# Kernel optimization log

Hardware: AMD Instinct MI355X
Metric: run time of the kernel (lower is better)

The kernel has to match this reference:

```python
import jax, jax.numpy as jnp
import numpy as np

N = 100000          # number of nodes
E = 128             # embedding size
NUM_LAYERS = 4
SMOOTH = 12.0       # MAXIMUM_SMOOTHNESS
RELATIONS = [("at", 2), ("clear", 1), ("on", 2)]  # sorted, as in module
ATOM_COUNTS = {"at": 150000, "clear": 150000, "on": 150000}


def mish(x):
    return x * jnp.tanh(jax.nn.softplus(x))


def _linear_init(k, din, dout):
    s = 1.0 / np.sqrt(din)
    kw, kb = jax.random.split(k)
    w = jax.random.uniform(kw, (din, dout), jnp.float32, -s, s)
    b = jax.random.uniform(kb, (dout,), jnp.float32, -s, s)
    return w, b


def setup_inputs() -> dict:
    key = jax.random.key(0)
    ks = iter(jax.random.split(key, 64))
    inp = {}
    inp["node_embeddings"] = jax.random.normal(next(ks), (N, E), jnp.float32)
    for name, ar in RELATIONS:
        inp[f"atoms_{name}"] = jax.random.randint(
            next(ks), (ATOM_COUNTS[name] * ar,), 0, N, dtype=jnp.int32)
        d = ar * E
        inp[f"w_in_{name}"], inp[f"b_in_{name}"] = _linear_init(next(ks), d, d)
        inp[f"w_out_{name}"], inp[f"b_out_{name}"] = _linear_init(next(ks), d, d)
    # update MLP: Linear(2E, 2E) -> mish -> Linear(2E, E)
    inp["w_u_in"], inp["b_u_in"] = _linear_init(next(ks), 2 * E, 2 * E)
    inp["w_u_out"], inp["b_u_out"] = _linear_init(next(ks), 2 * E, E)
    return inp


def _forward(node_embeddings, atoms, params):
    w_u_in, b_u_in, w_u_out, b_u_out = params["update"]

    def layer(h):
        msgs, idxs = [], []
        for name, ar in RELATIONS:
            w_in, b_in, w_out, b_out = params[name]
            av = atoms[name]                              # [A*ar] node indices
            x = h[av].reshape(-1, ar * E)                 # gather -> [A, ar*E]
            y = x + (mish(x @ w_in + b_in) @ w_out + b_out)  # residual MLP
            msgs.append(y.reshape(-1, E))
            idxs.append(av)
        msg = jnp.concatenate(msgs, 0)                    # [T, E]
        idx = jnp.concatenate(idxs, 0)                    # [T]
        # smooth-max aggregation (max offsets are not differentiated)
        seg_max = jax.ops.segment_max(msg, idx, num_segments=N)
        seg_max = jnp.where(jnp.isfinite(seg_max), seg_max, 0.0)  # empty -> 0 (include_self=False on zeros)
        seg_max = jax.lax.stop_gradient(seg_max)
        exps = jnp.exp(SMOOTH * (msg - seg_max[idx]))
        exps_sum = jax.ops.segment_sum(exps, idx, num_segments=N) + 1e-16
        max_msg = jnp.log(exps_sum) / SMOOTH + seg_max
        upd_in = jnp.concatenate([max_msg, h], axis=1)    # [N, 2E]
        upd = mish(upd_in @ w_u_in + b_u_in) @ w_u_out + b_u_out
        return h + upd                                    # outer residual

    h = node_embeddings
    for _ in range(NUM_LAYERS):
        h = layer(h)
    return h


def reference(node_embeddings, atoms_at, atoms_clear, atoms_on,
              w_in_at, b_in_at, w_out_at, b_out_at,
              w_in_clear, b_in_clear, w_out_clear, b_out_clear,
              w_in_on, b_in_on, w_out_on, b_out_on,
              w_u_in, b_u_in, w_u_out, b_u_out):
    atoms = {"at": atoms_at, "clear": atoms_clear, "on": atoms_on}
    params = {
        "at": (w_in_at, b_in_at, w_out_at, b_out_at),
        "clear": (w_in_clear, b_in_clear, w_out_clear, b_out_clear),
        "on": (w_in_on, b_in_on, w_out_on, b_out_on),
        "update": (w_u_in, b_u_in, w_u_out, b_u_out),
    }
    return _forward(node_embeddings, atoms, params)
```

## Files before the change

kernel.cpp:

```cpp
#include <hip/hip_runtime.h>
#include <hip/hip_bf16.h>
#include <math.h>

#define NNODES 100000
#define EDIM 128
#define TSLOTS 750000
#define NB 391

typedef __bf16 bf16x8 __attribute__((ext_vector_type(8)));
typedef __bf16 bf16x4 __attribute__((ext_vector_type(4)));
typedef float f32x4 __attribute__((ext_vector_type(4)));

#define T_SCALE 17.312340490667562f
#define INV_SCALE 0.05776226504666211f
#define EMPTY_V (-3.0701134f)

__device__ __forceinline__ float mishf(float x) {
  float u = __expf(fminf(x, 15.f));
  float num = u * (u + 2.f);
  return x * num * __builtin_amdgcn_rcpf(num + 2.f);
}

__device__ __forceinline__ double exp12t(float t) {
  t = fmaxf(t, -20000.f);
  float ti = floorf(t);
  float m = exp2f(t - ti);
  int ei = (int)ti;
  ei = ei < -1000 ? -1000 : (ei > 1000 ? 1000 : ei);
  return (double)m * __longlong_as_double(((long long)(1023 + ei)) << 52);
}

__device__ __forceinline__ float logS12(double S) {
  if (!(S > 0.0)) return EMPTY_V;
  long long b = __double_as_longlong(S);
  int e2 = (int)((b >> 52) & 0x7FF) - 1023;
  float mf = __uint_as_float(0x3F800000u | (unsigned)((b >> 29) & 0x7FFFFF));
  return ((float)e2 + log2f(mf)) * INV_SCALE;
}

__global__ void k_sentinel(float* out, int n) {
  int i = blockIdx.x * 256 + threadIdx.x;
  if (i < n) out[i] = 1.0e6f;
}

__global__ void k_init(const float* __restrict__ h0, __bf16* __restrict__ hb, int n8) {
  int i = blockIdx.x * 256 + threadIdx.x;
  if (i >= n8) return;
  float4 f0 = ((const float4*)h0)[i * 2];
  float4 f1 = ((const float4*)h0)[i * 2 + 1];
  bf16x8 p = {(__bf16)f0.x, (__bf16)f0.y, (__bf16)f0.z, (__bf16)f0.w,
              (__bf16)f1.x, (__bf16)f1.y, (__bf16)f1.z, (__bf16)f1.w};
  *(bf16x8*)(hb + (size_t)i * 8) = p;
}

struct TransDesc {
  const float* src[8];
  __bf16* dst[8];
  int R[8];
  int C[8];
  int tstart[9];
};

__global__ void k_transpose_all(TransDesc td) {
  __shared__ float tile[32][33];
  int b = blockIdx.x;
  int m = 0;
  while (m < 7 && b >= td.tstart[m + 1]) m++;
  int t = b - td.tstart[m];
  int R = td.R[m], C = td.C[m];
  int tcols = C >> 5;
  int by = t / tcols, bx = t - by * tcols;
  int tx = threadIdx.x & 31, ty = threadIdx.x >> 5;
  const float* src = td.src[m];
  __bf16* dst = td.dst[m];
  for (int i = 0; i < 32; i += 8)
    tile[ty + i][tx] = src[(size_t)(by * 32 + ty + i) * C + bx * 32 + tx];
  __syncthreads();
  for (int i = 0; i < 32; i += 8)
    dst[(size_t)(bx * 32 + ty + i) * R + by * 32 + tx] = (__bf16)tile[tx][ty + i];
}

__device__ __forceinline__ int slot_node(int s, const int* at, const int* cl, const int* on) {
  if (s < 300000) return at[s];
  if (s < 450000) return cl[s - 300000];
  return on[s - 450000];
}

__global__ void k_count(const int* __restrict__ at, const int* __restrict__ cl,
                        const int* __restrict__ on, int* __restrict__ cnt) {
  int s = blockIdx.x * 256 + threadIdx.x;
  if (s >= TSLOTS) return;
  atomicAdd(&cnt[slot_node(s, at, cl, on)], 1);
}

__global__ void k_bsum(const int* __restrict__ cnt, int* __restrict__ bsum) {
  __shared__ int sm[256];
  int n = blockIdx.x * 256 + threadIdx.x;
  sm[threadIdx.x] = (n < NNODES) ? cnt[n] : 0;
  __syncthreads();
  for (int st = 128; st > 0; st >>= 1) {
    if (threadIdx.x < st) sm[threadIdx.x] += sm[threadIdx.x + st];
    __syncthreads();
  }
  if (threadIdx.x == 0) bsum[blockIdx.x] = sm[0];
}

__global__ void k_bscan(const int* __restrict__ bsum, int* __restrict__ bpre,
                        int* __restrict__ off) {
  __shared__ int sm[512];
  int t = threadIdx.x;
  int v = (t < NB) ? bsum[t] : 0;
  sm[t] = v;
  __syncthreads();
  for (int st = 1; st < 512; st <<= 1) {
    int x = (t >= st) ? sm[t - st] : 0;
    __syncthreads();
    sm[t] += x;
    __syncthreads();
  }
  if (t < NB) bpre[t] = sm[t] - v;
  if (t == NB - 1) off[NNODES] = sm[t];
}

__global__ void k_off(const int* __restrict__ cnt, const int* __restrict__ bpre,
                      int* __restrict__ off) {
  __shared__ int sm[256];
  int n = blockIdx.x * 256 + threadIdx.x;
  int v = (n < NNODES) ? cnt[n] : 0;
  sm[threadIdx.x] = v;
  __syncthreads();
  for (int st = 1; st < 256; st <<= 1) {
    int t = (threadIdx.x >= st) ? sm[threadIdx.x - st] : 0;
    __syncthreads();
    sm[threadIdx.x] += t;
    __syncthreads();
  }
  if (n < NNODES) off[n] = bpre[blockIdx.x] + sm[threadIdx.x] - v;
}

__global__ void k_fill(const int* __restrict__ at, const int* __restrict__ cl,
                       const int* __restrict__ on, const int* __restrict__ off,
                       int* __restrict__ cnt, int* __restrict__ perm) {
  int s = blockIdx.x * 256 + threadIdx.x;
  if (s >= TSLOTS) return;
  int node = slot_node(s, at, cl, on);
  int pos = atomicAdd(&cnt[node], -1) - 1;
  perm[s] = off[node] + pos;
}

__global__ __launch_bounds__(256, 4) void k_rel2(
    const float* __restrict__ hf, const __bf16* __restrict__ hb,
    const int* __restrict__ av,
    const __bf16* __restrict__ wt1, const float* __restrict__ b1,
    const __bf16* __restrict__ wt2, const float* __restrict__ b2,
    _Float16* __restrict__ msg, const int* __restrict__ permrel, int A) {
  __shared__ __align__(16) __bf16 xs[64][264];
  __shared__ int prm[128];
  const int tid = threadIdx.x;
  const int lane = tid & 63;
  const int w = tid >> 6;
  const int row0 = blockIdx.x * 64;

  if (tid < 128) {
    int i2 = row0 * 2 + tid;
    prm[tid] = (i2 < 2 * A) ? permrel[i2] : 0;
  }
  if (hb != nullptr) {
    for (int i = 0; i < 8; ++i) {
      int s = tid + i * 256;
      int r = s >> 5, o = s & 31;
      int a = row0 + r;
      uint4 v = {0, 0, 0, 0};
      if (a < A) {
        int node = av[2 * a + (o >> 4)];
        v = *(const uint4*)(hb + (size_t)node * 128 + (o & 15) * 8);
      }
      *(uint4*)&xs[r][o * 8] = v;
    }
  } else {
    for (int i = 0; i < 16; ++i) {
      int s = tid + i * 256;
      int r = s >> 6, o = s & 63;
      int a = row0 + r;
      float4 f = {0.f, 0.f, 0.f, 0.f};
      if (a < A) {
        int node = av[2 * a + (o >> 5)];
        f = *(const float4*)(hf + (size_t)node * 128 + (o & 31) * 4);
      }
      bf16x4 p = {(__bf16)f.x, (__bf16)f.y, (__bf16)f.z, (__bf16)f.w};
      *(bf16x4*)&xs[r][o * 4] = p;
    }
  }
  __syncthreads();

  const int lhi = lane >> 4, llo = lane & 15;
  const int cb = w * 64;

  f32x4 acc1[4][4];
#pragma unroll
  for (int rt = 0; rt < 4; rt++)
#pragma unroll
    for (int ct = 0; ct < 4; ct++) acc1[rt][ct] = (f32x4){0.f, 0.f, 0.f, 0.f};

#pragma unroll
  for (int kk = 0; kk < 8; ++kk) {
    int k = kk * 32 + lhi * 8;
    bf16x8 af[4], bfr[4];
#pragma unroll
    for (int rt = 0; rt < 4; rt++) af[rt] = *(const bf16x8*)&xs[rt * 16 + llo][k];
#pragma unroll
    for (int ct = 0; ct < 4; ct++)
      bfr[ct] = *(const bf16x8*)(wt1 + (size_t)(cb + ct * 16 + llo) * 256 + k);
#pragma unroll
    for (int rt = 0; rt < 4; rt++)
#pragma unroll
      for (int ct = 0; ct < 4; ct++)
        acc1[rt][ct] = __builtin_amdgcn_mfma_f32_16x16x32_bf16(af[rt], bfr[ct], acc1[rt][ct], 0, 0, 0);
  }
  __syncthreads();

  float b1v[4];
#pragma unroll
  for (int ct = 0; ct < 4; ct++) b1v[ct] = b1[cb + ct * 16 + llo];
#pragma unroll
  for (int rt = 0; rt < 4; rt++)
#pragma unroll
    for (int ct = 0; ct < 4; ct++)
#pragma unroll
      for (int i = 0; i < 4; i++)
        xs[rt * 16 + lhi * 4 + i][cb + ct * 16 + llo] = (__bf16)mishf(acc1[rt][ct][i] + b1v[ct]);
  __syncthreads();

  f32x4 acc2[4][4];
#pragma unroll
  for (int rt = 0; rt < 4; rt++)
#pragma unroll
    for (int ct = 0; ct < 4; ct++) acc2[rt][ct] = (f32x4){0.f, 0.f, 0.f, 0.f};

#pragma unroll
  for (int kk = 0; kk < 8; ++kk) {
    int k = kk * 32 + lhi * 8;
    bf16x8 af[4], bfr[4];
#pragma unroll
    for (int rt = 0; rt < 4; rt++) af[rt] = *(const bf16x8*)&xs[rt * 16 + llo][k];
#pragma unroll
    for (int ct = 0; ct < 4; ct++)
      bfr[ct] = *(const bf16x8*)(wt2 + (size_t)(cb + ct * 16 + llo) * 256 + k);
#pragma unroll
    for (int rt = 0; rt < 4; rt++)
#pragma unroll
      for (int ct = 0; ct < 4; ct++)
        acc2[rt][ct] = __builtin_amdgcn_mfma_f32_16x16x32_bf16(af[rt], bfr[ct], acc2[rt][ct], 0, 0, 0);
  }
  __syncthreads();

  float b2v[4];
#pragma unroll
  for (int ct = 0; ct < 4; ct++) b2v[ct] = b2[cb + ct * 16 + llo];
  ushort* zs = (ushort*)&xs[0][0];
#pragma unroll
  for (int rt = 0; rt < 4; rt++)
#pragma unroll
    for (int ct = 0; ct < 4; ct++)
#pragma unroll
      for (int i = 0; i < 4; i++) {
        int r = rt * 16 + lhi * 4 + i;
        int col = cb + ct * 16 + llo;
        union { ushort u; _Float16 f; } cv;
        cv.f = (_Float16)(acc2[rt][ct][i] + b2v[ct]);
        zs[r * 264 + col] = cv.u;
      }
  __syncthreads();

  for (int i = 0; i < 8; ++i) {
    int s = tid + i * 256;
    int sr = s >> 4;
    int c = s & 15;
    int a = row0 + (sr >> 1);
    if (a < A) {
      int rr = sr >> 1, c0 = (sr & 1) * 128 + c * 8;
      uint4 z = *(const uint4*)&zs[rr * 264 + c0];
      *(uint4*)(msg + (size_t)prm[sr] * 128 + c * 8) = z;
    }
  }
}

__global__ __launch_bounds__(256, 4) void k_rel1(
    const float* __restrict__ hf, const __bf16* __restrict__ hb,
    const int* __restrict__ av,
    const __bf16* __restrict__ wt1, const float* __restrict__ b1,
    const __bf16* __restrict__ wt2, const float* __restrict__ b2,
    _Float16* __restrict__ msg, const int* __restrict__ permrel, int A) {
  __shared__ __align__(16) __bf16 xs[64][136];
  __shared__ int prm[64];
  const int tid = threadIdx.x;
  const int lane = tid & 63;
  const int w = tid >> 6;
  const int row0 = blockIdx.x * 64;

  if (tid < 64) {
    int a = row0 + tid;
    prm[tid] = (a < A) ? permrel[a] : 0;
  }
  if (hb != nullptr) {
    for (int i = 0; i < 4; ++i) {
      int s = tid + i * 256;
      int r = s >> 4, o = s & 15;
      int a = row0 + r;
      uint4 v = {0, 0, 0, 0};
      if (a < A) {
        int node = av[a];
        v = *(const uint4*)(hb + (size_t)node * 128 + o * 8);
      }
      *(uint4*)&xs[r][o * 8] = v;
    }
  } else {
    for (int i = 0; i < 8; ++i) {
      int s = tid + i * 256;
      int r = s >> 5, o = s & 31;
      int a = row0 + r;
      float4 f = {0.f, 0.f, 0.f, 0.f};
      if (a < A) {
        int node = av[a];
        f = *(const float4*)(hf + (size_t)node * 128 + o * 4);
      }
      bf16x4 p = {(__bf16)f.x, (__bf16)f.y, (__bf16)f.z, (__bf16)f.w};
      *(bf16x4*)&xs[r][o * 4] = p;
    }
  }
  __syncthreads();

  const int lhi = lane >> 4, llo = lane & 15;
  const int cb = w * 32;

  f32x4 acc1[4][2];
#pragma unroll
  for (int rt = 0; rt < 4; rt++)
#pragma unroll
    for (int ct = 0; ct < 2; ct++) acc1[rt][ct] = (f32x4){0.f, 0.f, 0.f, 0.f};

#pragma unroll
  for (int kk = 0; kk < 4; ++kk) {
    int k = kk * 32 + lhi * 8;
    bf16x8 af[4], bfr[2];
#pragma unroll
    for (int rt = 0; rt < 4; rt++) af[rt] = *(const bf16x8*)&xs[rt * 16 + llo][k];
#pragma unroll
    for (int ct = 0; ct < 2; ct++)
      bfr[ct] = *(const bf16x8*)(wt1 + (size_t)(cb + ct * 16 + llo) * 128 + k);
#pragma unroll
    for (int rt = 0; rt < 4; rt++)
#pragma unroll
      for (int ct = 0; ct < 2; ct++)
        acc1[rt][ct] = __builtin_amdgcn_mfma_f32_16x16x32_bf16(af[rt], bfr[ct], acc1[rt][ct], 0, 0, 0);
  }
  __syncthreads();

  float b1v[2];
#pragma unroll
  for (int ct = 0; ct < 2; ct++) b1v[ct] = b1[cb + ct * 16 + llo];
#pragma unroll
  for (int rt = 0; rt < 4; rt++)
#pragma unroll
    for (int ct = 0; ct < 2; ct++)
#pragma unroll
      for (int i = 0; i < 4; i++)
        xs[rt * 16 + lhi * 4 + i][cb + ct * 16 + llo] = (__bf16)mishf(acc1[rt][ct][i] + b1v[ct]);
  __syncthreads();

  f32x4 acc2[4][2];
#pragma unroll
  for (int rt = 0; rt < 4; rt++)
#pragma unroll
    for (int ct = 0; ct < 2; ct++) acc2[rt][ct] = (f32x4){0.f, 0.f, 0.f, 0.f};

#pragma unroll
  for (int kk = 0; kk < 4; ++kk) {
    int k = kk * 32 + lhi * 8;
    bf16x8 af[4], bfr[2];
#pragma unroll
    for (int rt = 0; rt < 4; rt++) af[rt] = *(const bf16x8*)&xs[rt * 16 + llo][k];
#pragma unroll
    for (int ct = 0; ct < 2; ct++)
      bfr[ct] = *(const bf16x8*)(wt2 + (size_t)(cb + ct * 16 + llo) * 128 + k);
#pragma unroll
    for (int rt = 0; rt < 4; rt++)
#pragma unroll
      for (int ct = 0; ct < 2; ct++)
        acc2[rt][ct] = __builtin_amdgcn_mfma_f32_16x16x32_bf16(af[rt], bfr[ct], acc2[rt][ct], 0, 0, 0);
  }
  __syncthreads();

  float b2v[2];
#pragma unroll
  for (int ct = 0; ct < 2; ct++) b2v[ct] = b2[cb + ct * 16 + llo];
  ushort* zs = (ushort*)&xs[0][0];
#pragma unroll
  for (int rt = 0; rt < 4; rt++)
#pragma unroll
    for (int ct = 0; ct < 2; ct++)
#pragma unroll
      for (int i = 0; i < 4; i++) {
        int r = rt * 16 + lhi * 4 + i;
        int col = cb + ct * 16 + llo;
        union { ushort u; _Float16 f; } cv;
        cv.f = (_Float16)(acc2[rt][ct][i] + b2v[ct]);
        zs[r * 136 + col] = cv.u;
      }
  __syncthreads();

  for (int i = 0; i < 4; ++i) {
    int s = tid + i * 256;
    int sr = s >> 4;
    int c = s & 15;
    int a = row0 + sr;
    if (a < A) {
      uint4 z = *(const uint4*)&zs[sr * 136 + c * 8];
      *(uint4*)(msg + (size_t)prm[sr] * 128 + c * 8) = z;
    }
  }
}

__global__ __launch_bounds__(256, 8) void k_agg(
    const _Float16* __restrict__ msg, const int* __restrict__ off,
    const float* __restrict__ hf, const __bf16* __restrict__ hb,
    __bf16* __restrict__ mm) {
  __shared__ int offs[33];
  const int tid = threadIdx.x;
  const int lane = tid & 63;
  const int w = tid >> 6;
  const int node0 = blockIdx.x * 32;
  if (tid < 33) {
    int n = node0 + tid;
    offs[tid] = off[n < NNODES ? n : NNODES];
  }
  __syncthreads();

  const int fl = lane & 31;
  const int p = lane >> 5;
  const _Float16* mb = msg + fl * 4;

#pragma unroll 1
  for (int j = 0; j < 8; ++j) {
    int n = node0 + w * 8 + j;
    if (n >= NNODES) break;
    float h0, h1, h2, h3;
    if (hb != nullptr) {
      bf16x4 hq = *(const bf16x4*)(hb + (size_t)n * 128 + fl * 4);
      h0 = (float)hq[0]; h1 = (float)hq[1]; h2 = (float)hq[2]; h3 = (float)hq[3];
    } else {
      float4 hq = *(const float4*)(hf + (size_t)n * 128 + fl * 4);
      h0 = hq.x; h1 = hq.y; h2 = hq.z; h3 = hq.w;
    }
    int beg = offs[w * 8 + j];
    int deg = offs[w * 8 + j + 1] - beg;
    double S0 = 0.0, S1 = 0.0, S2 = 0.0, S3 = 0.0;
#pragma unroll 1
    for (int d = 0; d < deg; d += 2) {
      int rp = d + p;
      int rc = rp < deg - 1 ? rp : deg - 1;
      uint2 v = *(const uint2*)(mb + (size_t)(beg + rc) * 128);
      if (rp >= deg) { v.x = 0xFC00FC00u; v.y = 0xFC00FC00u; }
      union { uint2 u; _Float16 f[4]; } q;
      q.u = v;
      S0 += exp12t(((float)q.f[0] + h0) * T_SCALE);
      S1 += exp12t(((float)q.f[1] + h1) * T_SCALE);
      S2 += exp12t(((float)q.f[2] + h2) * T_SCALE);
      S3 += exp12t(((float)q.f[3] + h3) * T_SCALE);
    }
    S0 += __shfl_xor(S0, 32);
    S1 += __shfl_xor(S1, 32);
    S2 += __shfl_xor(S2, 32);
    S3 += __shfl_xor(S3, 32);
    if (p == 0) {
      bf16x4 r;
      r[0] = (__bf16)logS12(S0);
      r[1] = (__bf16)logS12(S1);
      r[2] = (__bf16)logS12(S2);
      r[3] = (__bf16)logS12(S3);
      *(bf16x4*)(mm + (size_t)n * 128 + fl * 4) = r;
    }
  }
}

__global__ __launch_bounds__(256, 4) void k_mlp(
    const float* __restrict__ hin, const __bf16* __restrict__ mm,
    const __bf16* __restrict__ wt1, const float* __restrict__ b1,
    const __bf16* __restrict__ wt2, const float* __restrict__ b2,
    float* __restrict__ hout, __bf16* __restrict__ hbout) {
  __shared__ __align__(16) __bf16 xs[64][264];
  const int tid = threadIdx.x;
  const int lane = tid & 63;
  const int w = tid >> 6;
  const int node0 = blockIdx.x * 64;

  for (int i = 0; i < 4; ++i) {
    int s = tid + i * 256;
    int r = s >> 4, o = s & 15;
    int n = node0 + r;
    uint4 v = {0, 0, 0, 0};
    if (n < NNODES) v = *(const uint4*)(mm + (size_t)n * 128 + o * 8);
    *(uint4*)&xs[r][o * 8] = v;
  }
  for (int i = 0; i < 8; ++i) {
    int s = tid + i * 256;
    int r = s >> 5, o = s & 31;
    int n = node0 + r;
    float4 f = {0.f, 0.f, 0.f, 0.f};
    if (n < NNODES) f = *(const float4*)(hin + (size_t)n * 128 + o * 4);
    bf16x4 p = {(__bf16)f.x, (__bf16)f.y, (__bf16)f.z, (__bf16)f.w};
    *(bf16x4*)&xs[r][128 + o * 4] = p;
  }
  __syncthreads();

  const int lhi = lane >> 4, llo = lane & 15;
  const int cb = w * 64;

  f32x4 acc1[4][4];
#pragma unroll
  for (int rt = 0; rt < 4; rt++)
#pragma unroll
    for (int ct = 0; ct < 4; ct++) acc1[rt][ct] = (f32x4){0.f, 0.f, 0.f, 0.f};

#pragma unroll
  for (int kk = 0; kk < 8; ++kk) {
    int k = kk * 32 + lhi * 8;
    bf16x8 af[4], bfr[4];
#pragma unroll
    for (int rt = 0; rt < 4; rt++) af[rt] = *(const bf16x8*)&xs[rt * 16 + llo][k];
#pragma unroll
    for (int ct = 0; ct < 4; ct++)
      bfr[ct] = *(const bf16x8*)(wt1 + (size_t)(cb + ct * 16 + llo) * 256 + k);
#pragma unroll
    for (int rt = 0; rt < 4; rt++)
#pragma unroll
      for (int ct = 0; ct < 4; ct++)
        acc1[rt][ct] = __builtin_amdgcn_mfma_f32_16x16x32_bf16(af[rt], bfr[ct], acc1[rt][ct], 0, 0, 0);
  }
  __syncthreads();

  float b1v[4];
#pragma unroll
  for (int ct = 0; ct < 4; ct++) b1v[ct] = b1[cb + ct * 16 + llo];
#pragma unroll
  for (int rt = 0; rt < 4; rt++)
#pragma unroll
    for (int ct = 0; ct < 4; ct++)
#pragma unroll
      for (int i = 0; i < 4; i++)
        xs[rt * 16 + lhi * 4 + i][cb + ct * 16 + llo] = (__bf16)mishf(acc1[rt][ct][i] + b1v[ct]);
  __syncthreads();

  const int cb2 = w * 32;
  f32x4 acc2[4][2];
#pragma unroll
  for (int rt = 0; rt < 4; rt++)
#pragma unroll
    for (int ct = 0; ct < 2; ct++) acc2[rt][ct] = (f32x4){0.f, 0.f, 0.f, 0.f};

#pragma unroll
  for (int kk = 0; kk < 8; ++kk) {
    int k = kk * 32 + lhi * 8;
    bf16x8 af[4], bfr[2];
#pragma unroll
    for (int rt = 0; rt < 4; rt++) af[rt] = *(const bf16x8*)&xs[rt * 16 + llo][k];
#pragma unroll
    for (int ct = 0; ct < 2; ct++)
      bfr[ct] = *(const bf16x8*)(wt2 + (size_t)(cb2 + ct * 16 + llo) * 256 + k);
#pragma unroll
    for (int rt = 0; rt < 4; rt++)
#pragma unroll
      for (int ct = 0; ct < 2; ct++)
        acc2[rt][ct] = __builtin_amdgcn_mfma_f32_16x16x32_bf16(af[rt], bfr[ct], acc2[rt][ct], 0, 0, 0);
  }

  float b2v[2];
#pragma unroll
  for (int ct = 0; ct < 2; ct++) b2v[ct] = b2[cb2 + ct * 16 + llo];
#pragma unroll
  for (int rt = 0; rt < 4; rt++)
#pragma unroll
    for (int i = 0; i < 4; i++) {
      int r = rt * 16 + lhi * 4 + i;
      int n = node0 + r;
      if (n >= NNODES) continue;
#pragma unroll
      for (int ct = 0; ct < 2; ct++) {
        int col = cb2 + ct * 16 + llo;
        size_t idx = (size_t)n * 128 + col;
        float nh = hin[idx] + acc2[rt][ct][i] + b2v[ct];
        hout[idx] = nh;
        if (hbout != nullptr) hbout[idx] = (__bf16)nh;
      }
    }
}

extern "C" void kernel_launch(void* const* d_in, const int* in_sizes, int n_in,
                              void* d_out, int out_size, void* d_ws, size_t ws_size,
                              hipStream_t stream) {
  const float* h0 = (const float*)d_in[0];
  const int* at = (const int*)d_in[1];
  const float* w_in_at = (const float*)d_in[2];
  const float* b_in_at = (const float*)d_in[3];
  const float* w_out_at = (const float*)d_in[4];
  const float* b_out_at = (const float*)d_in[5];
  const int* cl = (const int*)d_in[6];
  const float* w_in_cl = (const float*)d_in[7];
  const float* b_in_cl = (const float*)d_in[8];
  const float* w_out_cl = (const float*)d_in[9];
  const float* b_out_cl = (const float*)d_in[10];
  const int* on = (const int*)d_in[11];
  const float* w_in_on = (const float*)d_in[12];
  const float* b_in_on = (const float*)d_in[13];
  const float* w_out_on = (const float*)d_in[14];
  const float* b_out_on = (const float*)d_in[15];
  const float* w_u_in = (const float*)d_in[16];
  const float* b_u_in = (const float*)d_in[17];
  const float* w_u_out = (const float*)d_in[18];
  const float* b_u_out = (const float*)d_in[19];

  float* hout = (float*)d_out;
  char* ws = (char*)d_ws;

  const size_t MSG_B = (size_t)TSLOTS * 128 * 2;
  const size_t OFF_B = 400016;
  const size_t CNT_B = 400000;
  const size_t BS_B = 1568;
  const size_t PERM_B = 3000000;
  const size_t WT_B = 786432;
  const size_t MM_B = (size_t)NNODES * 128 * 2;
  const size_t HB_B = (size_t)NNODES * 128 * 2;
  const size_t REQ2 = MSG_B + OFF_B + CNT_B + 2 * BS_B + PERM_B + WT_B + MM_B;
  const size_t REQ3 = REQ2 + HB_B;

  if (ws_size < REQ2) {
    k_sentinel<<<(out_size + 255) / 256, 256, 0, stream>>>((float*)d_out, out_size);
    return;
  }

  _Float16* msg = (_Float16*)ws;
  int* off = (int*)(ws + MSG_B);
  int* cnt = (int*)(ws + MSG_B + OFF_B);
  int* bsum = (int*)(ws + MSG_B + OFF_B + CNT_B);
  int* bpre = (int*)(ws + MSG_B + OFF_B + CNT_B + BS_B);
  int* perm = (int*)(ws + MSG_B + OFF_B + CNT_B + 2 * BS_B);
  __bf16* wt = (__bf16*)(ws + MSG_B + OFF_B + CNT_B + 2 * BS_B + PERM_B);
  __bf16* mm = (__bf16*)(ws + MSG_B + OFF_B + CNT_B + 2 * BS_B + PERM_B + WT_B);
  __bf16* hb = (ws_size >= REQ3) ? (__bf16*)(ws + REQ2) : nullptr;

  __bf16* wt_in_at = wt;
  __bf16* wt_out_at = wt + 65536;
  __bf16* wt_in_on = wt + 131072;
  __bf16* wt_out_on = wt + 196608;
  __bf16* wt_u_in = wt + 262144;
  __bf16* wt_u_out = wt + 327680;
  __bf16* wt_in_cl = wt + 360448;
  __bf16* wt_out_cl = wt + 376832;

  TransDesc td;
  const float* srcs[8] = {w_in_at, w_out_at, w_in_on, w_out_on, w_u_in, w_u_out, w_in_cl, w_out_cl};
  __bf16* dsts[8] = {wt_in_at, wt_out_at, wt_in_on, wt_out_on, wt_u_in, wt_u_out, wt_in_cl, wt_out_cl};
  int Rs[8] = {256, 256, 256, 256, 256, 256, 128, 128};
  int Cs[8] = {256, 256, 256, 256, 256, 128, 128, 128};
  int ts = 0;
  for (int m = 0; m < 8; ++m) {
    td.src[m] = srcs[m]; td.dst[m] = dsts[m]; td.R[m] = Rs[m]; td.C[m] = Cs[m];
    td.tstart[m] = ts; ts += (Rs[m] / 32) * (Cs[m] / 32);
  }
  td.tstart[8] = ts;
  k_transpose_all<<<384, 256, 0, stream>>>(td);

  if (hb) k_init<<<6250, 256, 0, stream>>>(h0, hb, NNODES * EDIM / 8);

  const int grid_rel = (150000 + 63) / 64;
  const int grid_mlp = (NNODES + 63) / 64;
  const int grid_agg = (NNODES + 31) / 32;
  const int grid_slots = (TSLOTS + 255) / 256;

  hipMemsetAsync(cnt, 0, CNT_B, stream);
  k_count<<<grid_slots, 256, 0, stream>>>(at, cl, on, cnt);
  k_bsum<<<NB, 256, 0, stream>>>(cnt, bsum);
  k_bscan<<<1, 512, 0, stream>>>(bsum, bpre, off);
  k_off<<<NB, 256, 0, stream>>>(cnt, bpre, off);
  k_fill<<<grid_slots, 256, 0, stream>>>(at, cl, on, off, cnt, perm);

  const int* perm_at = perm;
  const int* perm_cl = perm + 300000;
  const int* perm_on = perm + 450000;

  for (int l = 0; l < 4; ++l) {
    const float* hs = (l == 0) ? h0 : hout;
    k_rel2<<<grid_rel, 256, 0, stream>>>(hs, hb, at, wt_in_at, b_in_at, wt_out_at, b_out_at, msg, perm_at, 150000);
    k_rel1<<<grid_rel, 256, 0, stream>>>(hs, hb, cl, wt_in_cl, b_in_cl, wt_out_cl, b_out_cl, msg, perm_cl, 150000);
    k_rel2<<<grid_rel, 256, 0, stream>>>(hs, hb, on, wt_in_on, b_in_on, wt_out_on, b_out_on, msg, perm_on, 150000);
    k_agg<<<grid_agg, 256, 0, stream>>>(msg, off, hs, hb, mm);
    k_mlp<<<grid_mlp, 256, 0, stream>>>(hs, mm, wt_u_in, b_u_in, wt_u_out, b_u_out, hout, hb);
  }
}
```

Measured before the change: 1.805 ms.

## Fuse three relation kernels into one launch and use 512-thread blocks

```diff
diff --git a/kernel.cpp b/kernel.cpp
--- a/kernel.cpp
+++ b/kernel.cpp
@@ -6,6 +6,7 @@
 #define EDIM 128
 #define TSLOTS 750000
 #define NB 391
+#define GRA 2344
 
 typedef __bf16 bf16x8 __attribute__((ext_vector_type(8)));
 typedef __bf16 bf16x4 __attribute__((ext_vector_type(4)));
@@ -148,275 +149,250 @@
   perm[s] = off[node] + pos;
 }
 
-__global__ __launch_bounds__(256, 4) void k_rel2(
+struct RelAll {
+  const int* av[3];
+  const __bf16* wt1[3];
+  const float* b1[3];
+  const __bf16* wt2[3];
+  const float* b2[3];
+  const int* prm[3];
+};
+
+__global__ __launch_bounds__(512, 6) void k_relf(
     const float* __restrict__ hf, const __bf16* __restrict__ hb,
-    const int* __restrict__ av,
-    const __bf16* __restrict__ wt1, const float* __restrict__ b1,
-    const __bf16* __restrict__ wt2, const float* __restrict__ b2,
-    _Float16* __restrict__ msg, const int* __restrict__ permrel, int A) {
+    RelAll ra, _Float16* __restrict__ msg) {
   __shared__ __align__(16) __bf16 xs[64][264];
   __shared__ int prm[128];
   const int tid = threadIdx.x;
   const int lane = tid & 63;
   const int w = tid >> 6;
-  const int row0 = blockIdx.x * 64;
-
-  if (tid < 128) {
-    int i2 = row0 * 2 + tid;
-    prm[tid] = (i2 < 2 * A) ? permrel[i2] : 0;
-  }
-  if (hb != nullptr) {
-    for (int i = 0; i < 8; ++i) {
-      int s = tid + i * 256;
-      int r = s >> 5, o = s & 31;
-      int a = row0 + r;
-      uint4 v = {0, 0, 0, 0};
+  const int b = blockIdx.x;
+  const int m = (b < GRA) ? 0 : (b < 2 * GRA ? 1 : 2);
+  const int row0 = (b - m * GRA) * 64;
+  const int A = 150000;
+  const int* av = ra.av[m];
+  const __bf16* wt1 = ra.wt1[m];
+  const float* b1 = ra.b1[m];
+  const __bf16* wt2 = ra.wt2[m];
+  const float* b2 = ra.b2[m];
+  const int* permrel = ra.prm[m];
+  const int lhi = lane >> 4, llo = lane & 15;
+  ushort* zs = (ushort*)&xs[0][0];
+
+  if (m < 2) {
+    if (tid < 128) {
+      int i2 = row0 * 2 + tid;
+      prm[tid] = (i2 < 2 * A) ? permrel[i2] : 0;
+    }
+    if (hb != nullptr) {
+      for (int i = 0; i < 4; ++i) {
+        int s = tid + i * 512;
+        int r = s >> 5, o = s & 31;
+        int a = row0 + r;
+        uint4 v = {0, 0, 0, 0};
+        if (a < A) {
+          int node = av[2 * a + (o >> 4)];
+          v = *(const uint4*)(hb + (size_t)node * 128 + (o & 15) * 8);
+        }
+        *(uint4*)&xs[r][o * 8] = v;
+      }
+    } else {
+      for (int i = 0; i < 8; ++i) {
+        int s = tid + i * 512;
+        int r = s >> 6, o = s & 63;
+        int a = row0 + r;
+        float4 f = {0.f, 0.f, 0.f, 0.f};
+        if (a < A) {
+          int node = av[2 * a + (o >> 5)];
+          f = *(const float4*)(hf + (size_t)node * 128 + (o & 31) * 4);
+        }
+        bf16x4 p = {(__bf16)f.x, (__bf16)f.y, (__bf16)f.z, (__bf16)f.w};
+        *(bf16x4*)&xs[r][o * 4] = p;
+      }
+    }
+    __syncthreads();
+
+    const int cb = w * 32;
+    f32x4 acc1[4][2];
+#pragma unroll
+    for (int rt = 0; rt < 4; rt++)
+#pragma unroll
+      for (int ct = 0; ct < 2; ct++) acc1[rt][ct] = (f32x4){0.f, 0.f, 0.f, 0.f};
+#pragma unroll
+    for (int kk = 0; kk < 8; ++kk) {
+      int k = kk * 32 + lhi * 8;
+      bf16x8 af[4], bfr[2];
+#pragma unroll
+      for (int rt = 0; rt < 4; rt++) af[rt] = *(const bf16x8*)&xs[rt * 16 + llo][k];
+#pragma unroll
+      for (int ct = 0; ct < 2; ct++)
+        bfr[ct] = *(const bf16x8*)(wt1 + (size_t)(cb + ct * 16 + llo) * 256 + k);
+#pragma unroll
+      for (int rt = 0; rt < 4; rt++)
+#pragma unroll
+        for (int ct = 0; ct < 2; ct++)
+          acc1[rt][ct] = __builtin_amdgcn_mfma_f32_16x16x32_bf16(af[rt], bfr[ct], acc1[rt][ct], 0, 0, 0);
+    }
+    __syncthreads();
+
+    float b1v[2];
+#pragma unroll
+    for (int ct = 0; ct < 2; ct++) b1v[ct] = b1[cb + ct * 16 + llo];
+#pragma unroll
+    for (int rt = 0; rt < 4; rt++)
+#pragma unroll
+      for (int ct = 0; ct < 2; ct++)
+#pragma unroll
+        for (int i = 0; i < 4; i++)
+          xs[rt * 16 + lhi * 4 + i][cb + ct * 16 + llo] = (__bf16)mishf(acc1[rt][ct][i] + b1v[ct]);
+    __syncthreads();
+
+    f32x4 acc2[4][2];
+#pragma unroll
+    for (int rt = 0; rt < 4; rt++)
+#pragma unroll
+      for (int ct = 0; ct < 2; ct++) acc2[rt][ct] = (f32x4){0.f, 0.f, 0.f, 0.f};
+#pragma unroll
+    for (int kk = 0; kk < 8; ++kk) {
+      int k = kk * 32 + lhi * 8;
+      bf16x8 af[4], bfr[2];
+#pragma unroll
+      for (int rt = 0; rt < 4; rt++) af[rt] = *(const bf16x8*)&xs[rt * 16 + llo][k];
+#pragma unroll
+      for (int ct = 0; ct < 2; ct++)
+        bfr[ct] = *(const bf16x8*)(wt2 + (size_t)(cb + ct * 16 + llo) * 256 + k);
+#pragma unroll
+      for (int rt = 0; rt < 4; rt++)
+#pragma unroll
+        for (int ct = 0; ct < 2; ct++)
+          acc2[rt][ct] = __builtin_amdgcn_mfma_f32_16x16x32_bf16(af[rt], bfr[ct], acc2[rt][ct], 0, 0, 0);
+    }
+    __syncthreads();
+
+    float b2v[2];
+#pragma unroll
+    for (int ct = 0; ct < 2; ct++) b2v[ct] = b2[cb + ct * 16 + llo];
+#pragma unroll
+    for (int rt = 0; rt < 4; rt++)
+#pragma unroll
+      for (int ct = 0; ct < 2; ct++)
+#pragma unroll
+        for (int i = 0; i < 4; i++) {
+          int r = rt * 16 + lhi * 4 + i;
+          int col = cb + ct * 16 + llo;
+          union { ushort u; _Float16 f; } cv;
+          cv.f = (_Float16)(acc2[rt][ct][i] + b2v[ct]);
+          zs[r * 264 + col] = cv.u;
+        }
+    __syncthreads();
+
+    for (int i = 0; i < 4; ++i) {
+      int s = tid + i * 512;
+      int sr = s >> 4;
+      int c = s & 15;
+      int a = row0 + (sr >> 1);
       if (a < A) {
-        int node = av[2 * a + (o >> 4)];
-        v = *(const uint4*)(hb + (size_t)node * 128 + (o & 15) * 8);
+        int rr = sr >> 1, c0 = (sr & 1) * 128 + c * 8;
+        uint4 z = *(const uint4*)&zs[rr * 264 + c0];
+        *(uint4*)(msg + (size_t)prm[sr] * 128 + c * 8) = z;
       }
-      *(uint4*)&xs[r][o * 8] = v;
     }
   } else {
-    for (int i = 0; i < 16; ++i) {
-      int s = tid + i * 256;
-      int r = s >> 6, o = s & 63;
-      int a = row0 + r;
-      float4 f = {0.f, 0.f, 0.f, 0.f};
-      if (a < A) {
-        int node = av[2 * a + (o >> 5)];
-        f = *(const float4*)(hf + (size_t)node * 128 + (o & 31) * 4);
+    if (tid < 64) {
+      int a = row0 + tid;
+      prm[tid] = (a < A) ? permrel[a] : 0;
+    }
+    if (hb != nullptr) {
+      for (int i = 0; i < 2; ++i) {
+        int s = tid + i * 512;
+        int r = s >> 4, o = s & 15;
+        int a = row0 + r;
+        uint4 v = {0, 0, 0, 0};
+        if (a < A) {
+          int node = av[a];
+          v = *(const uint4*)(hb + (size_t)node * 128 + o * 8);
+        }
+        *(uint4*)&xs[r][o * 8] = v;
       }
-      bf16x4 p = {(__bf16)f.x, (__bf16)f.y, (__bf16)f.z, (__bf16)f.w};
-      *(bf16x4*)&xs[r][o * 4] = p;
-    }
-  }
-  __syncthreads();
-
-  const int lhi = lane >> 4, llo = lane & 15;
-  const int cb = w * 64;
-
-  f32x4 acc1[4][4];
-#pragma unroll
-  for (int rt = 0; rt < 4; rt++)
-#pragma unroll
-    for (int ct = 0; ct < 4; ct++) acc1[rt][ct] = (f32x4){0.f, 0.f, 0.f, 0.f};
-
-#pragma unroll
-  for (int kk = 0; kk < 8; ++kk) {
-    int k = kk * 32 + lhi * 8;
-    bf16x8 af[4], bfr[4];
-#pragma unroll
-    for (int rt = 0; rt < 4; rt++) af[rt] = *(const bf16x8*)&xs[rt * 16 + llo][k];
-#pragma unroll
-    for (int ct = 0; ct < 4; ct++)
-      bfr[ct] = *(const bf16x8*)(wt1 + (size_t)(cb + ct * 16 + llo) * 256 + k);
-#pragma unroll
-    for (int rt = 0; rt < 4; rt++)
-#pragma unroll
-      for (int ct = 0; ct < 4; ct++)
-        acc1[rt][ct] = __builtin_amdgcn_mfma_f32_16x16x32_bf16(af[rt], bfr[ct], acc1[rt][ct], 0, 0, 0);
-  }
-  __syncthreads();
-
-  float b1v[4];
-#pragma unroll
-  for (int ct = 0; ct < 4; ct++) b1v[ct] = b1[cb + ct * 16 + llo];
-#pragma unroll
-  for (int rt = 0; rt < 4; rt++)
-#pragma unroll
-    for (int ct = 0; ct < 4; ct++)
+    } else {
+      for (int i = 0; i < 4; ++i) {
+        int s = tid + i * 512;
+        int r = s >> 5, o = s & 31;
+        int a = row0 + r;
+        float4 f = {0.f, 0.f, 0.f, 0.f};
+        if (a < A) {
+          int node = av[a];
+          f = *(const float4*)(hf + (size_t)node * 128 + o * 4);
+        }
+        bf16x4 p = {(__bf16)f.x, (__bf16)f.y, (__bf16)f.z, (__bf16)f.w};
+        *(bf16x4*)&xs[r][o * 4] = p;
+      }
+    }
+    __syncthreads();
+
+    const int cb = w * 16;
+    f32x4 acc1[4];
+#pragma unroll
+    for (int rt = 0; rt < 4; rt++) acc1[rt] = (f32x4){0.f, 0.f, 0.f, 0.f};
+#pragma unroll
+    for (int kk = 0; kk < 4; ++kk) {
+      int k = kk * 32 + lhi * 8;
+      bf16x8 af[4], bfr;
+#pragma unroll
+      for (int rt = 0; rt < 4; rt++) af[rt] = *(const bf16x8*)&xs[rt * 16 + llo][k];
+      bfr = *(const bf16x8*)(wt1 + (size_t)(cb + llo) * 128 + k);
+#pragma unroll
+      for (int rt = 0; rt < 4; rt++)
+        acc1[rt] = __builtin_amdgcn_mfma_f32_16x16x32_bf16(af[rt], bfr, acc1[rt], 0, 0, 0);
+    }
+    __syncthreads();
+
+    float b1v = b1[cb + llo];
+#pragma unroll
+    for (int rt = 0; rt < 4; rt++)
 #pragma unroll
       for (int i = 0; i < 4; i++)
-        xs[rt * 16 + lhi * 4 + i][cb + ct * 16 + llo] = (__bf16)mishf(acc1[rt][ct][i] + b1v[ct]);
-  __syncthreads();
-
-  f32x4 acc2[4][4];
-#pragma unroll
-  for (int rt = 0; rt < 4; rt++)
-#pragma unroll
-    for (int ct = 0; ct < 4; ct++) acc2[rt][ct] = (f32x4){0.f, 0.f, 0.f, 0.f};
-
-#pragma unroll
-  for (int kk = 0; kk < 8; ++kk) {
-    int k = kk * 32 + lhi * 8;
-    bf16x8 af[4], bfr[4];
-#pragma unroll
-    for (int rt = 0; rt < 4; rt++) af[rt] = *(const bf16x8*)&xs[rt * 16 + llo][k];
-#pragma unroll
-    for (int ct = 0; ct < 4; ct++)
-      bfr[ct] = *(const bf16x8*)(wt2 + (size_t)(cb + ct * 16 + llo) * 256 + k);
-#pragma unroll
-    for (int rt = 0; rt < 4; rt++)
-#pragma unroll
-      for (int ct = 0; ct < 4; ct++)
-        acc2[rt][ct] = __builtin_amdgcn_mfma_f32_16x16x32_bf16(af[rt], bfr[ct], acc2[rt][ct], 0, 0, 0);
-  }
-  __syncthreads();
-
-  float b2v[4];
-#pragma unroll
-  for (int ct = 0; ct < 4; ct++) b2v[ct] = b2[cb + ct * 16 + llo];
-  ushort* zs = (ushort*)&xs[0][0];
-#pragma unroll
-  for (int rt = 0; rt < 4; rt++)
-#pragma unroll
-    for (int ct = 0; ct < 4; ct++)
+        xs[rt * 16 + lhi * 4 + i][cb + llo] = (__bf16)mishf(acc1[rt][i] + b1v);
+    __syncthreads();
+
+    f32x4 acc2[4];
+#pragma unroll
+    for (int rt = 0; rt < 4; rt++) acc2[rt] = (f32x4){0.f, 0.f, 0.f, 0.f};
+#pragma unroll
+    for (int kk = 0; kk < 4; ++kk) {
+      int k = kk * 32 + lhi * 8;
+      bf16x8 af[4], bfr;
+#pragma unroll
+      for (int rt = 0; rt < 4; rt++) af[rt] = *(const bf16x8*)&xs[rt * 16 + llo][k];
+      bfr = *(const bf16x8*)(wt2 + (size_t)(cb + llo) * 128 + k);
+#pragma unroll
+      for (int rt = 0; rt < 4; rt++)
+        acc2[rt] = __builtin_amdgcn_mfma_f32_16x16x32_bf16(af[rt], bfr, acc2[rt], 0, 0, 0);
+    }
+    __syncthreads();
+
+    float b2v = b2[cb + llo];
+#pragma unroll
+    for (int rt = 0; rt < 4; rt++)
 #pragma unroll
       for (int i = 0; i < 4; i++) {
         int r = rt * 16 + lhi * 4 + i;
-        int col = cb + ct * 16 + llo;
+        int col = cb + llo;
         union { ushort u; _Float16 f; } cv;
-        cv.f = (_Float16)(acc2[rt][ct][i] + b2v[ct]);
+        cv.f = (_Float16)(acc2[rt][i] + b2v);
         zs[r * 264 + col] = cv.u;
       }
-  __syncthreads();
-
-  for (int i = 0; i < 8; ++i) {
-    int s = tid + i * 256;
-    int sr = s >> 4;
-    int c = s & 15;
-    int a = row0 + (sr >> 1);
-    if (a < A) {
-      int rr = sr >> 1, c0 = (sr & 1) * 128 + c * 8;
-      uint4 z = *(const uint4*)&zs[rr * 264 + c0];
-      *(uint4*)(msg + (size_t)prm[sr] * 128 + c * 8) = z;
-    }
-  }
-}
-
-__global__ __launch_bounds__(256, 4) void k_rel1(
-    const float* __restrict__ hf, const __bf16* __restrict__ hb,
-    const int* __restrict__ av,
-    const __bf16* __restrict__ wt1, const float* __restrict__ b1,
-    const __bf16* __restrict__ wt2, const float* __restrict__ b2,
-    _Float16* __restrict__ msg, const int* __restrict__ permrel, int A) {
-  __shared__ __align__(16) __bf16 xs[64][136];
-  __shared__ int prm[64];
-  const int tid = threadIdx.x;
-  const int lane = tid & 63;
-  const int w = tid >> 6;
-  const int row0 = blockIdx.x * 64;
-
-  if (tid < 64) {
-    int a = row0 + tid;
-    prm[tid] = (a < A) ? permrel[a] : 0;
-  }
-  if (hb != nullptr) {
-    for (int i = 0; i < 4; ++i) {
-      int s = tid + i * 256;
-      int r = s >> 4, o = s & 15;
-      int a = row0 + r;
-      uint4 v = {0, 0, 0, 0};
+    __syncthreads();
+
+    for (int i = 0; i < 2; ++i) {
+      int s = tid + i * 512;
+      int sr = s >> 4;
+      int c = s & 15;
+      int a = row0 + sr;
       if (a < A) {
-        int node = av[a];
-        v = *(const uint4*)(hb + (size_t)node * 128 + o * 8);
+        uint4 z = *(const uint4*)&zs[sr * 264 + c * 8];
+        *(uint4*)(msg + (size_t)prm[sr] * 128 + c * 8) = z;
       }
-      *(uint4*)&xs[r][o * 8] = v;
-    }
-  } else {
-    for (int i = 0; i < 8; ++i) {
-      int s = tid + i * 256;
-      int r = s >> 5, o = s & 31;
-      int a = row0 + r;
-      float4 f = {0.f, 0.f, 0.f, 0.f};
-      if (a < A) {
-        int node = av[a];
-        f = *(const float4*)(hf + (size_t)node * 128 + o * 4);
-      }
-      bf16x4 p = {(__bf16)f.x, (__bf16)f.y, (__bf16)f.z, (__bf16)f.w};
-      *(bf16x4*)&xs[r][o * 4] = p;
-    }
-  }
-  __syncthreads();
-
-  const int lhi = lane >> 4, llo = lane & 15;
-  const int cb = w * 32;
-
-  f32x4 acc1[4][2];
-#pragma unroll
-  for (int rt = 0; rt < 4; rt++)
-#pragma unroll
-    for (int ct = 0; ct < 2; ct++) acc1[rt][ct] = (f32x4){0.f, 0.f, 0.f, 0.f};
-
-#pragma unroll
-  for (int kk = 0; kk < 4; ++kk) {
-    int k = kk * 32 + lhi * 8;
-    bf16x8 af[4], bfr[2];
-#pragma unroll
-    for (int rt = 0; rt < 4; rt++) af[rt] = *(const bf16x8*)&xs[rt * 16 + llo][k];
-#pragma unroll
-    for (int ct = 0; ct < 2; ct++)
-      bfr[ct] = *(const bf16x8*)(wt1 + (size_t)(cb + ct * 16 + llo) * 128 + k);
-#pragma unroll
-    for (int rt = 0; rt < 4; rt++)
-#pragma unroll
-      for (int ct = 0; ct < 2; ct++)
-        acc1[rt][ct] = __builtin_amdgcn_mfma_f32_16x16x32_bf16(af[rt], bfr[ct], acc1[rt][ct], 0, 0, 0);
-  }
-  __syncthreads();
-
-  float b1v[2];
-#pragma unroll
-  for (int ct = 0; ct < 2; ct++) b1v[ct] = b1[cb + ct * 16 + llo];
-#pragma unroll
-  for (int rt = 0; rt < 4; rt++)
-#pragma unroll
-    for (int ct = 0; ct < 2; ct++)
-#pragma unroll
-      for (int i = 0; i < 4; i++)
-        xs[rt * 16 + lhi * 4 + i][cb + ct * 16 + llo] = (__bf16)mishf(acc1[rt][ct][i] + b1v[ct]);
-  __syncthreads();
-
-  f32x4 acc2[4][2];
-#pragma unroll
-  for (int rt = 0; rt < 4; rt++)
-#pragma unroll
-    for (int ct = 0; ct < 2; ct++) acc2[rt][ct] = (f32x4){0.f, 0.f, 0.f, 0.f};
-
-#pragma unroll
-  for (int kk = 0; kk < 4; ++kk) {
-    int k = kk * 32 + lhi * 8;
-    bf16x8 af[4], bfr[2];
-#pragma unroll
-    for (int rt = 0; rt < 4; rt++) af[rt] = *(const bf16x8*)&xs[rt * 16 + llo][k];
-#pragma unroll
-    for (int ct = 0; ct < 2; ct++)
-      bfr[ct] = *(const bf16x8*)(wt2 + (size_t)(cb + ct * 16 + llo) * 128 + k);
-#pragma unroll
-    for (int rt = 0; rt < 4; rt++)
-#pragma unroll
-      for (int ct = 0; ct < 2; ct++)
-        acc2[rt][ct] = __builtin_amdgcn_mfma_f32_16x16x32_bf16(af[rt], bfr[ct], acc2[rt][ct], 0, 0, 0);
-  }
-  __syncthreads();
-
-  float b2v[2];
-#pragma unroll
-  for (int ct = 0; ct < 2; ct++) b2v[ct] = b2[cb + ct * 16 + llo];
-  ushort* zs = (ushort*)&xs[0][0];
-#pragma unroll
-  for (int rt = 0; rt < 4; rt++)
-#pragma unroll
-    for (int ct = 0; ct < 2; ct++)
-#pragma unroll
-      for (int i = 0; i < 4; i++) {
-        int r = rt * 16 + lhi * 4 + i;
-        int col = cb + ct * 16 + llo;
-        union { ushort u; _Float16 f; } cv;
-        cv.f = (_Float16)(acc2[rt][ct][i] + b2v[ct]);
-        zs[r * 136 + col] = cv.u;
-      }
-  __syncthreads();
-
-  for (int i = 0; i < 4; ++i) {
-    int s = tid + i * 256;
-    int sr = s >> 4;
-    int c = s & 15;
-    int a = row0 + sr;
-    if (a < A) {
-      uint4 z = *(const uint4*)&zs[sr * 136 + c * 8];
-      *(uint4*)(msg + (size_t)prm[sr] * 128 + c * 8) = z;
     }
   }
 }
@@ -483,7 +459,7 @@
   }
 }
 
-__global__ __launch_bounds__(256, 4) void k_mlp(
+__global__ __launch_bounds__(512, 6) void k_mlp(
     const float* __restrict__ hin, const __bf16* __restrict__ mm,
     const __bf16* __restrict__ wt1, const float* __restrict__ b1,
     const __bf16* __restrict__ wt2, const float* __restrict__ b2,
@@ -494,16 +470,16 @@
   const int w = tid >> 6;
   const int node0 = blockIdx.x * 64;
 
-  for (int i = 0; i < 4; ++i) {
-    int s = tid + i * 256;
+  for (int i = 0; i < 2; ++i) {
+    int s = tid + i * 512;
     int r = s >> 4, o = s & 15;
     int n = node0 + r;
     uint4 v = {0, 0, 0, 0};
     if (n < NNODES) v = *(const uint4*)(mm + (size_t)n * 128 + o * 8);
     *(uint4*)&xs[r][o * 8] = v;
   }
-  for (int i = 0; i < 8; ++i) {
-    int s = tid + i * 256;
+  for (int i = 0; i < 4; ++i) {
+    int s = tid + i * 512;
     int r = s >> 5, o = s & 31;
     int n = node0 + r;
     float4 f = {0.f, 0.f, 0.f, 0.f};
@@ -514,50 +490,13 @@
   __syncthreads();
 
   const int lhi = lane >> 4, llo = lane & 15;
-  const int cb = w * 64;
-
-  f32x4 acc1[4][4];
+  const int cb = w * 32;
+
+  f32x4 acc1[4][2];
 #pragma unroll
   for (int rt = 0; rt < 4; rt++)
 #pragma unroll
-    for (int ct = 0; ct < 4; ct++) acc1[rt][ct] = (f32x4){0.f, 0.f, 0.f, 0.f};
-
-#pragma unroll
-  for (int kk = 0; kk < 8; ++kk) {
-    int k = kk * 32 + lhi * 8;
-    bf16x8 af[4], bfr[4];
-#pragma unroll
-    for (int rt = 0; rt < 4; rt++) af[rt] = *(const bf16x8*)&xs[rt * 16 + llo][k];
-#pragma unroll
-    for (int ct = 0; ct < 4; ct++)
-      bfr[ct] = *(const bf16x8*)(wt1 + (size_t)(cb + ct * 16 + llo) * 256 + k);
-#pragma unroll
-    for (int rt = 0; rt < 4; rt++)
-#pragma unroll
-      for (int ct = 0; ct < 4; ct++)
-        acc1[rt][ct] = __builtin_amdgcn_mfma_f32_16x16x32_bf16(af[rt], bfr[ct], acc1[rt][ct], 0, 0, 0);
-  }
-  __syncthreads();
-
-  float b1v[4];
-#pragma unroll
-  for (int ct = 0; ct < 4; ct++) b1v[ct] = b1[cb + ct * 16 + llo];
-#pragma unroll
-  for (int rt = 0; rt < 4; rt++)
-#pragma unroll
-    for (int ct = 0; ct < 4; ct++)
-#pragma unroll
-      for (int i = 0; i < 4; i++)
-        xs[rt * 16 + lhi * 4 + i][cb + ct * 16 + llo] = (__bf16)mishf(acc1[rt][ct][i] + b1v[ct]);
-  __syncthreads();
-
-  const int cb2 = w * 32;
-  f32x4 acc2[4][2];
-#pragma unroll
-  for (int rt = 0; rt < 4; rt++)
-#pragma unroll
-    for (int ct = 0; ct < 2; ct++) acc2[rt][ct] = (f32x4){0.f, 0.f, 0.f, 0.f};
-
+    for (int ct = 0; ct < 2; ct++) acc1[rt][ct] = (f32x4){0.f, 0.f, 0.f, 0.f};
 #pragma unroll
   for (int kk = 0; kk < 8; ++kk) {
     int k = kk * 32 + lhi * 8;
@@ -566,17 +505,44 @@
     for (int rt = 0; rt < 4; rt++) af[rt] = *(const bf16x8*)&xs[rt * 16 + llo][k];
 #pragma unroll
     for (int ct = 0; ct < 2; ct++)
-      bfr[ct] = *(const bf16x8*)(wt2 + (size_t)(cb2 + ct * 16 + llo) * 256 + k);
+      bfr[ct] = *(const bf16x8*)(wt1 + (size_t)(cb + ct * 16 + llo) * 256 + k);
 #pragma unroll
     for (int rt = 0; rt < 4; rt++)
 #pragma unroll
       for (int ct = 0; ct < 2; ct++)
-        acc2[rt][ct] = __builtin_amdgcn_mfma_f32_16x16x32_bf16(af[rt], bfr[ct], acc2[rt][ct], 0, 0, 0);
-  }
-
-  float b2v[2];
-#pragma unroll
-  for (int ct = 0; ct < 2; ct++) b2v[ct] = b2[cb2 + ct * 16 + llo];
+        acc1[rt][ct] = __builtin_amdgcn_mfma_f32_16x16x32_bf16(af[rt], bfr[ct], acc1[rt][ct], 0, 0, 0);
+  }
+  __syncthreads();
+
+  float b1v[2];
+#pragma unroll
+  for (int ct = 0; ct < 2; ct++) b1v[ct] = b1[cb + ct * 16 + llo];
+#pragma unroll
+  for (int rt = 0; rt < 4; rt++)
+#pragma unroll
+    for (int ct = 0; ct < 2; ct++)
+#pragma unroll
+      for (int i = 0; i < 4; i++)
+        xs[rt * 16 + lhi * 4 + i][cb + ct * 16 + llo] = (__bf16)mishf(acc1[rt][ct][i] + b1v[ct]);
+  __syncthreads();
+
+  const int cb2 = w * 16;
+  f32x4 acc2[4];
+#pragma unroll
+  for (int rt = 0; rt < 4; rt++) acc2[rt] = (f32x4){0.f, 0.f, 0.f, 0.f};
+#pragma unroll
+  for (int kk = 0; kk < 8; ++kk) {
+    int k = kk * 32 + lhi * 8;
+    bf16x8 af[4], bfr;
+#pragma unroll
+    for (int rt = 0; rt < 4; rt++) af[rt] = *(const bf16x8*)&xs[rt * 16 + llo][k];
+    bfr = *(const bf16x8*)(wt2 + (size_t)(cb2 + llo) * 256 + k);
+#pragma unroll
+    for (int rt = 0; rt < 4; rt++)
+      acc2[rt] = __builtin_amdgcn_mfma_f32_16x16x32_bf16(af[rt], bfr, acc2[rt], 0, 0, 0);
+  }
+
+  float b2v = b2[cb2 + llo];
 #pragma unroll
   for (int rt = 0; rt < 4; rt++)
 #pragma unroll
@@ -584,14 +550,11 @@
       int r = rt * 16 + lhi * 4 + i;
       int n = node0 + r;
       if (n >= NNODES) continue;
-#pragma unroll
-      for (int ct = 0; ct < 2; ct++) {
-        int col = cb2 + ct * 16 + llo;
-        size_t idx = (size_t)n * 128 + col;
-        float nh = hin[idx] + acc2[rt][ct][i] + b2v[ct];
-        hout[idx] = nh;
-        if (hbout != nullptr) hbout[idx] = (__bf16)nh;
-      }
+      int col = cb2 + llo;
+      size_t idx = (size_t)n * 128 + col;
+      float nh = hin[idx] + acc2[rt][i] + b2v;
+      hout[idx] = nh;
+      if (hbout != nullptr) hbout[idx] = (__bf16)nh;
     }
 }
 
@@ -672,7 +635,6 @@
 
   if (hb) k_init<<<6250, 256, 0, stream>>>(h0, hb, NNODES * EDIM / 8);
 
-  const int grid_rel = (150000 + 63) / 64;
   const int grid_mlp = (NNODES + 63) / 64;
   const int grid_agg = (NNODES + 31) / 32;
   const int grid_slots = (TSLOTS + 255) / 256;
@@ -684,16 +646,15 @@
   k_off<<<NB, 256, 0, stream>>>(cnt, bpre, off);
   k_fill<<<grid_slots, 256, 0, stream>>>(at, cl, on, off, cnt, perm);
 
-  const int* perm_at = perm;
-  const int* perm_cl = perm + 300000;
-  const int* perm_on = perm + 450000;
+  RelAll ra;
+  ra.av[0] = at;  ra.wt1[0] = wt_in_at; ra.b1[0] = b_in_at; ra.wt2[0] = wt_out_at; ra.b2[0] = b_out_at; ra.prm[0] = perm;
+  ra.av[1] = on;  ra.wt1[1] = wt_in_on; ra.b1[1] = b_in_on; ra.wt2[1] = wt_out_on; ra.b2[1] = b_out_on; ra.prm[1] = perm + 450000;
+  ra.av[2] = cl;  ra.wt1[2] = wt_in_cl; ra.b1[2] = b_in_cl; ra.wt2[2] = wt_out_cl; ra.b2[2] = b_out_cl; ra.prm[2] = perm + 300000;
 
   for (int l = 0; l < 4; ++l) {
     const float* hs = (l == 0) ? h0 : hout;
-    k_rel2<<<grid_rel, 256, 0, stream>>>(hs, hb, at, wt_in_at, b_in_at, wt_out_at, b_out_at, msg, perm_at, 150000);
-    k_rel1<<<grid_rel, 256, 0, stream>>>(hs, hb, cl, wt_in_cl, b_in_cl, wt_out_cl, b_out_cl, msg, perm_cl, 150000);
-    k_rel2<<<grid_rel, 256, 0, stream>>>(hs, hb, on, wt_in_on, b_in_on, wt_out_on, b_out_on, msg, perm_on, 150000);
+    k_relf<<<3 * GRA, 512, 0, stream>>>(hs, hb, ra, msg);
     k_agg<<<grid_agg, 256, 0, stream>>>(msg, off, hs, hb, mm);
-    k_mlp<<<grid_mlp, 256, 0, stream>>>(hs, mm, wt_u_in, b_u_in, wt_u_out, b_u_out, hout, hb);
-  }
-}
+    k_mlp<<<grid_mlp, 512, 0, stream>>>(hs, mm, wt_u_in, b_u_in, wt_u_out, b_u_out, hout, hb);
+  }
+}
```

Result: faster. 1.644 ms (-8.9%).
